# Kernel tuning notes

Hardware: AMD Instinct MI355X
Metric: run time of the kernel (lower is better)

## Reference

```python
import jax, jax.numpy as jnp
import numpy as np

B, T, D = 2, 2048, 512
HEADS, DIM_HEAD, MAX_LAG = 8, 64, 5
INNER = HEADS * DIM_HEAD


def setup_inputs() -> dict:
    key = jax.random.key(0)
    k0, k1, k2, k3, k4 = jax.random.split(key, 5)
    x = jax.random.normal(k0, (B, T, D), dtype=jnp.float32)
    # Linear weights stored as (in, out); torch applies x @ W.T with W (out, in).
    Wq = jax.random.normal(k1, (D, INNER), dtype=jnp.float32) * (1.0 / np.sqrt(D))
    Wk = jax.random.normal(k2, (D, INNER), dtype=jnp.float32) * (1.0 / np.sqrt(D))
    Wv = jax.random.normal(k3, (D, INNER), dtype=jnp.float32) * (1.0 / np.sqrt(D))
    Wo = jax.random.normal(k4, (INNER, D), dtype=jnp.float32) * (1.0 / np.sqrt(INNER))
    bo = jnp.zeros((D,), dtype=jnp.float32)
    # Module's init: lag_weights = log(exp(-lags/(max_lag/3))) = -lags/(max_lag/3)
    lags = jnp.arange(MAX_LAG + 1, dtype=jnp.float32)
    lag_weights = jnp.broadcast_to(-(lags / (MAX_LAG / 3.0)), (HEADS, MAX_LAG + 1)).astype(jnp.float32)
    return {"x": x, "Wq": Wq, "Wk": Wk, "Wv": Wv, "Wo": Wo, "bo": bo, "lag_weights": lag_weights}


def reference(x, Wq, Wk, Wv, Wo, bo, lag_weights):
    b, t, _ = x.shape
    h, dh = HEADS, DIM_HEAD
    scale = dh ** -0.5
    # context defaults to x (self-attention)
    q = (x @ Wq).reshape(b, t, h, dh).transpose(0, 2, 1, 3)  # b h t d
    k = (x @ Wk).reshape(b, t, h, dh).transpose(0, 2, 1, 3)
    v = (x @ Wv).reshape(b, t, h, dh).transpose(0, 2, 1, 3)
    sim = jnp.einsum('bhid,bhjd->bhij', q, k) * scale  # b h t t
    # causal mask: keep j <= i
    causal = jnp.tril(jnp.ones((t, t), dtype=bool))
    neg = -jnp.finfo(sim.dtype).max
    sim = jnp.where(causal[None, None], sim, neg)
    # learned additive time-lag bias: lag_adj[h,i,j] = softmax(lag_weights)[h, clamp(i-j,0,MAX_LAG)]
    ti = jnp.arange(t)
    time_lags = jnp.clip(ti[:, None] - ti[None, :], 0, MAX_LAG)  # t t
    lag_probs = jax.nn.softmax(lag_weights, axis=-1)  # h (L+1)
    lag_adj = lag_probs[:, time_lags]  # h t t
    sim = sim + lag_adj[None]
    attn = jax.nn.softmax(sim, axis=-1)
    out = jnp.einsum('bhij,bhjd->bhid', attn, v)
    out = out.transpose(0, 2, 1, 3).reshape(b, t, h * dh)  # b t inner
    return out @ Wo + bo  # dropout is identity at eval
```

## Files before the change

### kernel.cpp

```cpp
#include <hip/hip_runtime.h>
#include <hip/hip_bf16.h>

#define BB 2
#define TT 2048
#define DD 512
#define HH 8
#define DH 64
#define INNER 512
#define MAXLAG 5

typedef __attribute__((ext_vector_type(8))) short short8;
typedef __attribute__((ext_vector_type(4))) float floatx4;
typedef unsigned short ushort_t;

__device__ inline unsigned short f2bf(float f) {
    unsigned u = __float_as_uint(f);
    unsigned r = (u + 0x7FFFu + ((u >> 16) & 1u)) >> 16;
    return (unsigned short)r;
}
__device__ inline float bf2f(unsigned short u) {
    return __uint_as_float(((unsigned)u) << 16);
}

#define NXE (BB * TT * DD)

__global__ __launch_bounds__(256)
void cvt_kernel(const float* __restrict__ x,
                const float* __restrict__ wq, const float* __restrict__ wk,
                const float* __restrict__ wv, const float* __restrict__ wo,
                ushort_t* __restrict__ xb,
                ushort_t* __restrict__ wqt, ushort_t* __restrict__ wkt,
                ushort_t* __restrict__ wvt, ushort_t* __restrict__ wot)
{
    __shared__ float T[32][33];
    const int bid = blockIdx.x;
    if (bid < 1024) {
        int off = (bid * 256 + threadIdx.x) * 8;
        float4 a = *(const float4*)&x[off];
        float4 b = *(const float4*)&x[off + 4];
        ushort_t t[8];
        t[0] = f2bf(a.x); t[1] = f2bf(a.y); t[2] = f2bf(a.z); t[3] = f2bf(a.w);
        t[4] = f2bf(b.x); t[5] = f2bf(b.y); t[6] = f2bf(b.z); t[7] = f2bf(b.w);
        *(uint4*)&xb[off] = *(const uint4*)t;
        return;
    }
    const int r = bid - 1024;
    const int z = r >> 8;
    const int tile = r & 255;
    const float* s = (z == 0) ? wq : (z == 1) ? wk : (z == 2) ? wv : wo;
    ushort_t*    d = (z == 0) ? wqt : (z == 1) ? wkt : (z == 2) ? wvt : wot;
    const int k0 = (tile & 15) * 32;
    const int n0 = (tile >> 4) * 32;
    {
        const int kk = threadIdx.x >> 3;
        const int n4 = (threadIdx.x & 7) * 4;
        float4 v = *(const float4*)&s[(size_t)(k0 + kk) * 512 + n0 + n4];
        T[kk][n4 + 0] = v.x; T[kk][n4 + 1] = v.y;
        T[kk][n4 + 2] = v.z; T[kk][n4 + 3] = v.w;
    }
    __syncthreads();
    {
        const int nn = threadIdx.x >> 3;
        const int k4 = (threadIdx.x & 7) * 4;
        ushort4 o;
        o.x = f2bf(T[k4 + 0][nn]); o.y = f2bf(T[k4 + 1][nn]);
        o.z = f2bf(T[k4 + 2][nn]); o.w = f2bf(T[k4 + 3][nn]);
        *(ushort4*)&d[(size_t)(n0 + nn) * 512 + k0 + k4] = o;
    }
}

#define GM 64
#define GN 64
#define GK 32

template <typename OutT>
__global__ __launch_bounds__(256)
void gemm64(const ushort_t* __restrict__ A,
            const ushort_t* __restrict__ B0, const ushort_t* __restrict__ B1,
            const ushort_t* __restrict__ B2,
            OutT* __restrict__ O0, OutT* __restrict__ O1, OutT* __restrict__ O2,
            const float* __restrict__ bias, int M, int N, int K, int vtrans)
{
    const ushort_t* Bw = (blockIdx.z == 0) ? B0 : ((blockIdx.z == 1) ? B1 : B2);
    OutT*           O  = (blockIdx.z == 0) ? O0 : ((blockIdx.z == 1) ? O1 : O2);
    const int dotrans = vtrans && (blockIdx.z == 2);

    __shared__ ushort_t As[GM * GK];
    __shared__ ushort_t Bs[GN * GK];

    const int tid  = threadIdx.x;
    const int wave = tid >> 6;
    const int lane = tid & 63;
    const int quad = lane >> 4;
    const int l15  = lane & 15;
    const int wr   = wave >> 1;
    const int wc   = wave & 1;
    const int bm   = blockIdx.y * GM;
    const int bn   = blockIdx.x * GN;

    const ushort_t* ap = &A[(size_t)(bm + (tid >> 2)) * K + (tid & 3) * 8];
    const ushort_t* bp = &Bw[(size_t)(bn + (tid >> 2)) * K + (tid & 3) * 8];

    floatx4 acc[2][2];
#pragma unroll
    for (int i = 0; i < 2; ++i)
#pragma unroll
        for (int j = 0; j < 2; ++j) acc[i][j] = (floatx4){0.f, 0.f, 0.f, 0.f};

    uint4 pa = *(const uint4*)ap;
    uint4 pb = *(const uint4*)bp;

    for (int k0 = 0; k0 < K; k0 += GK) {
        __syncthreads();
        *(uint4*)&As[tid * 8] = pa;
        *(uint4*)&Bs[tid * 8] = pb;
        if (k0 + GK < K) {
            pa = *(const uint4*)(ap + k0 + GK);
            pb = *(const uint4*)(bp + k0 + GK);
        }
        __syncthreads();

        short8 af[2], bf[2];
#pragma unroll
        for (int mt = 0; mt < 2; ++mt)
            af[mt] = *(const short8*)&As[(((wr * 32 + mt * 16 + l15) << 2) + quad) * 8];
#pragma unroll
        for (int nt = 0; nt < 2; ++nt)
            bf[nt] = *(const short8*)&Bs[(((wc * 32 + nt * 16 + l15) << 2) + quad) * 8];
#pragma unroll
        for (int mt = 0; mt < 2; ++mt)
#pragma unroll
            for (int nt = 0; nt < 2; ++nt)
                acc[mt][nt] = __builtin_amdgcn_mfma_f32_16x16x32_bf16(
                    af[mt], bf[nt], acc[mt][nt], 0, 0, 0);
    }

    if (dotrans) {
#pragma unroll
        for (int mt = 0; mt < 2; ++mt) {
            const int m0 = bm + wr * 32 + mt * 16 + quad * 4;
            const int b  = m0 >> 11;
            const int t0 = m0 & 2047;
#pragma unroll
            for (int nt = 0; nt < 2; ++nt) {
                const int n = bn + wc * 32 + nt * 16 + l15;
                const int h = n >> 6, dd = n & 63;
                ushort4 o;
                o.x = f2bf(acc[mt][nt][0]); o.y = f2bf(acc[mt][nt][1]);
                o.z = f2bf(acc[mt][nt][2]); o.w = f2bf(acc[mt][nt][3]);
                *(ushort4*)&((ushort_t*)O)[((size_t)((b * 8 + h) * 64 + dd)) * 2048 + t0] = o;
            }
        }
        return;
    }

    float bv[2] = {0.f, 0.f};
    if (bias) {
#pragma unroll
        for (int nt = 0; nt < 2; ++nt)
            bv[nt] = bias[bn + wc * 32 + nt * 16 + l15];
    }
#pragma unroll
    for (int mt = 0; mt < 2; ++mt) {
#pragma unroll
        for (int nt = 0; nt < 2; ++nt) {
            const int n = bn + wc * 32 + nt * 16 + l15;
#pragma unroll
            for (int reg = 0; reg < 4; ++reg) {
                const int m = bm + wr * 32 + mt * 16 + quad * 4 + reg;
                float v = acc[mt][nt][reg] + bv[nt];
                if constexpr (sizeof(OutT) == 2)
                    O[(size_t)m * N + n] = (OutT)f2bf(v);
                else
                    O[(size_t)m * N + n] = (OutT)v;
            }
        }
    }
}

#define PAD 72
#define MFIX 10.0f

__global__ __launch_bounds__(256)
void attn_mfma(const ushort_t* __restrict__ Qg,
               const ushort_t* __restrict__ Kg,
               const ushort_t* __restrict__ Vtg,
               const float* __restrict__ lagw,
               ushort_t* __restrict__ Opart,
               float* __restrict__ Lpart)
{
    __shared__ ushort_t Ks[64 * 8 * 8];
    __shared__ ushort_t Vts[64 * 8 * 8];
    __shared__ ushort_t Pl[4][16][PAD];

    const int tid  = threadIdx.x;
    const int wave = tid >> 6;
    const int lane = tid & 63;
    const int quad = lane >> 4;
    const int l15  = lane & 15;

    const int bh = blockIdx.y;
    const int b  = bh >> 3;
    const int h  = bh & 7;
    const int c  = blockIdx.x;
    const int qt = 31 - (c >> 1);
    const int sp = c & 1;
    const int i0 = qt * 64;
    const int h1 = (qt + 1) >> 1;
    const int lo = sp ? h1 : 0;
    const int hi = sp ? (qt + 1) : h1;

    float lagb[MAXLAG + 1];
    {
        float mx = -1e30f;
#pragma unroll
        for (int l = 0; l <= MAXLAG; ++l) {
            lagb[l] = lagw[h * (MAXLAG + 1) + l];
            mx = fmaxf(mx, lagb[l]);
        }
        float s = 0.f;
#pragma unroll
        for (int l = 0; l <= MAXLAG; ++l) { lagb[l] = __expf(lagb[l] - mx); s += lagb[l]; }
        float inv = 1.f / s;
#pragma unroll
        for (int l = 0; l <= MAXLAG; ++l) lagb[l] = lagb[l] * inv - MFIX;
    }
    const float c1  = 0.125f;
    const float c2f = lagb[MAXLAG];

    short8 qf0, qf1;
    {
        const ushort_t* qbase =
            Qg + ((size_t)(b * TT + i0 + wave * 16 + l15)) * INNER + h * DH;
        qf0 = *(const short8*)(qbase + quad * 8);
        qf1 = *(const short8*)(qbase + 32 + quad * 8);
    }

    floatx4 oacc[4];
    float lsum[4] = {0.f, 0.f, 0.f, 0.f};
#pragma unroll
    for (int cb = 0; cb < 4; ++cb) oacc[cb] = (floatx4){0.f, 0.f, 0.f, 0.f};

    const int ibase = i0 + wave * 16 + quad * 4;

    const int srow = tid >> 3;
    const int sc   = tid & 7;
    const ushort_t* Kp0 = Kg + ((size_t)(b * TT) + srow) * INNER + h * DH + sc * 8;
    const ushort_t* Kp1 = Kp0 + (size_t)32 * INNER;
    const ushort_t* Vp0 = Vtg + ((size_t)(bh * 64 + srow)) * 2048 + sc * 8;
    const ushort_t* Vp1 = Vp0 + (size_t)32 * 2048;
    const int slot = (sc + srow) & 7;
    const int kdst0 = ((srow << 3) + slot) << 3;
    const int kdst1 = (((srow + 32) << 3) + slot) << 3;

    uint4 pk0, pk1, pv0, pv1;
    if (lo < hi) {
        const size_t koff = (size_t)(lo * 64) * INNER;
        pk0 = *(const uint4*)(Kp0 + koff);
        pk1 = *(const uint4*)(Kp1 + koff);
        pv0 = *(const uint4*)(Vp0 + lo * 64);
        pv1 = *(const uint4*)(Vp1 + lo * 64);
    }

    for (int kt = lo; kt < hi; ++kt) {
        __syncthreads();
        *(uint4*)&Ks[kdst0]  = pk0;
        *(uint4*)&Ks[kdst1]  = pk1;
        *(uint4*)&Vts[kdst0] = pv0;
        *(uint4*)&Vts[kdst1] = pv1;
        if (kt + 1 < hi) {
            const size_t koff = (size_t)((kt + 1) * 64) * INNER;
            pk0 = *(const uint4*)(Kp0 + koff);
            pk1 = *(const uint4*)(Kp1 + koff);
            pv0 = *(const uint4*)(Vp0 + (kt + 1) * 64);
            pv1 = *(const uint4*)(Vp1 + (kt + 1) * 64);
        }
        __syncthreads();

        const int j0 = kt * 64;

        floatx4 sacc[4];
#pragma unroll
        for (int cb = 0; cb < 4; ++cb) {
            const int key = cb * 16 + l15;
            short8 kf0 = *(const short8*)&Ks[((key << 3) + ((quad + key) & 7)) << 3];
            short8 kf1 = *(const short8*)&Ks[((key << 3) + ((quad + 4 + key) & 7)) << 3];
            floatx4 z = (floatx4){0.f, 0.f, 0.f, 0.f};
            z = __builtin_amdgcn_mfma_f32_16x16x32_bf16(qf0, kf0, z, 0, 0, 0);
            z = __builtin_amdgcn_mfma_f32_16x16x32_bf16(qf1, kf1, z, 0, 0, 0);
            sacc[cb] = z;
        }

        float p[4][4];
        if (i0 + wave * 16 - (j0 + 63) >= MAXLAG) {
#pragma unroll
            for (int cb = 0; cb < 4; ++cb)
#pragma unroll
                for (int reg = 0; reg < 4; ++reg)
                    p[cb][reg] = __expf(fmaf(sacc[cb][reg], c1, c2f));
        } else {
#pragma unroll
            for (int cb = 0; cb < 4; ++cb) {
                const int j = j0 + cb * 16 + l15;
#pragma unroll
                for (int reg = 0; reg < 4; ++reg) {
                    const int lag = (ibase + reg) - j;
                    float bias = (lag <= 0) ? lagb[0]
                               : (lag == 1) ? lagb[1]
                               : (lag == 2) ? lagb[2]
                               : (lag == 3) ? lagb[3]
                               : (lag == 4) ? lagb[4] : lagb[5];
                    float e = __expf(fmaf(sacc[cb][reg], c1, bias));
                    p[cb][reg] = (lag < 0) ? 0.f : e;
                }
            }
        }
#pragma unroll
        for (int cb = 0; cb < 4; ++cb)
#pragma unroll
            for (int reg = 0; reg < 4; ++reg)
                lsum[reg] += p[cb][reg];

#pragma unroll
        for (int cb = 0; cb < 4; ++cb)
#pragma unroll
            for (int reg = 0; reg < 4; ++reg)
                Pl[wave][quad * 4 + reg][cb * 16 + l15] = f2bf(p[cb][reg]);

        short8 pf0 = *(const short8*)&Pl[wave][l15][quad * 8];
        short8 pf1 = *(const short8*)&Pl[wave][l15][32 + quad * 8];

#pragma unroll
        for (int cb = 0; cb < 4; ++cb) {
            const int dd = cb * 16 + l15;
            short8 vf0 = *(const short8*)&Vts[((dd << 3) + ((quad + dd) & 7)) << 3];
            short8 vf1 = *(const short8*)&Vts[((dd << 3) + ((quad + 4 + dd) & 7)) << 3];
            oacc[cb] = __builtin_amdgcn_mfma_f32_16x16x32_bf16(pf0, vf0, oacc[cb], 0, 0, 0);
            oacc[cb] = __builtin_amdgcn_mfma_f32_16x16x32_bf16(pf1, vf1, oacc[cb], 0, 0, 0);
        }
    }

#pragma unroll
    for (int reg = 0; reg < 4; ++reg) {
        lsum[reg] += __shfl_xor(lsum[reg], 1);
        lsum[reg] += __shfl_xor(lsum[reg], 2);
        lsum[reg] += __shfl_xor(lsum[reg], 4);
        lsum[reg] += __shfl_xor(lsum[reg], 8);
    }

#pragma unroll
    for (int reg = 0; reg < 4; ++reg) {
        const int row = ibase + reg;
        const size_t obase = ((size_t)(sp * 16 + bh) * TT + row) * 64;
#pragma unroll
        for (int cb = 0; cb < 4; ++cb)
            Opart[obase + cb * 16 + l15] = f2bf(oacc[cb][reg]);
        if (l15 == 0)
            Lpart[(size_t)(sp * 16 + bh) * TT + row] = lsum[reg];
    }
}

#define CMB_UNITS (16 * TT * 16)

__global__ __launch_bounds__(256)
void combine_kernel(const ushort_t* __restrict__ Opart,
                    const float* __restrict__ Lpart,
                    ushort_t* __restrict__ ao)
{
    int u = blockIdx.x * 256 + threadIdx.x;
    const int bh  = u >> 15;
    const int rem = u & 32767;
    const int i   = rem >> 4;
    const int d   = (rem & 15) * 4;
    const int b   = bh >> 3;
    const int h   = bh & 7;

    const size_t p0 = ((size_t)bh * TT + i) * 64 + d;
    const size_t p1 = ((size_t)(16 + bh) * TT + i) * 64 + d;
    ushort4 a0 = *(const ushort4*)&Opart[p0];
    ushort4 a1 = *(const ushort4*)&Opart[p1];
    const float l = Lpart[(size_t)bh * TT + i] + Lpart[(size_t)(16 + bh) * TT + i];
    const float inv = 1.f / l;

    ushort4 o;
    o.x = f2bf((bf2f(a0.x) + bf2f(a1.x)) * inv);
    o.y = f2bf((bf2f(a0.y) + bf2f(a1.y)) * inv);
    o.z = f2bf((bf2f(a0.z) + bf2f(a1.z)) * inv);
    o.w = f2bf((bf2f(a0.w) + bf2f(a1.w)) * inv);
    *(ushort4*)&ao[((size_t)(b * TT + i)) * INNER + h * DH + d] = o;
}

extern "C" void kernel_launch(void* const* d_in, const int* in_sizes, int n_in,
                              void* d_out, int out_size, void* d_ws, size_t ws_size,
                              hipStream_t stream)
{
    const float* x  = (const float*)d_in[0];
    const float* Wq = (const float*)d_in[1];
    const float* Wk = (const float*)d_in[2];
    const float* Wv = (const float*)d_in[3];
    const float* Wo = (const float*)d_in[4];
    const float* bo = (const float*)d_in[5];
    const float* lw = (const float*)d_in[6];
    float* out = (float*)d_out;

    const size_t SZ  = (size_t)BB * TT * INNER;
    const size_t NWE = (size_t)DD * INNER;
    ushort_t* xb    = (ushort_t*)d_ws;
    ushort_t* wqt   = xb + SZ;
    ushort_t* wkt   = wqt + NWE;
    ushort_t* wvt   = wkt + NWE;
    ushort_t* wot   = wvt + NWE;
    ushort_t* q     = wot + NWE;
    ushort_t* k     = q + SZ;
    ushort_t* vt    = k + SZ;
    ushort_t* opart = vt + SZ;
    float*    lpart = (float*)(opart + 2 * SZ);
    ushort_t* ao    = xb;

    const int M = BB * TT;

    cvt_kernel<<<2048, 256, 0, stream>>>(x, Wq, Wk, Wv, Wo,
                                         xb, wqt, wkt, wvt, wot);

    dim3 gQKV(INNER / GN, M / GM, 3);
    gemm64<ushort_t><<<gQKV, 256, 0, stream>>>(
        xb, wqt, wkt, wvt, q, k, vt, nullptr, M, INNER, DD, 1);

    dim3 gATT(64, BB * HH);
    attn_mfma<<<gATT, 256, 0, stream>>>(q, k, vt, lw, opart, lpart);

    combine_kernel<<<CMB_UNITS / 256, 256, 0, stream>>>(opart, lpart, ao);

    dim3 gPRJ(DD / GN, M / GM, 1);
    gemm64<float><<<gPRJ, 256, 0, stream>>>(
        ao, wot, wot, wot, out, out, out, bo, M, DD, INNER, 0);
}
```

Measured before the change: 138.6 us.

## Load K and V fragments directly from global memory, dropping LDS staging

The attention kernel stops staging K and V tiles through shared memory. Each wave now reads its MFMA operand fragments straight from global memory, prefetching the next K tile into registers and loading V at the start of each iteration. This removes the two block barriers per key tile and the LDS round trip. In exchange, every one of the four waves loads the same K/V data redundantly, relying on cache, and register pressure rises.

```diff
diff --git a/kernel.cpp b/kernel.cpp
--- a/kernel.cpp
+++ b/kernel.cpp
@@ -21,8 +21,6 @@
 __device__ inline float bf2f(unsigned short u) {
     return __uint_as_float(((unsigned)u) << 16);
 }
-
-#define NXE (BB * TT * DD)
 
 __global__ __launch_bounds__(256)
 void cvt_kernel(const float* __restrict__ x,
@@ -189,8 +187,6 @@
                ushort_t* __restrict__ Opart,
                float* __restrict__ Lpart)
 {
-    __shared__ ushort_t Ks[64 * 8 * 8];
-    __shared__ ushort_t Vts[64 * 8 * 8];
     __shared__ ushort_t Pl[4][16][PAD];
 
     const int tid  = threadIdx.x;
@@ -243,51 +239,51 @@
 
     const int ibase = i0 + wave * 16 + quad * 4;
 
-    const int srow = tid >> 3;
-    const int sc   = tid & 7;
-    const ushort_t* Kp0 = Kg + ((size_t)(b * TT) + srow) * INNER + h * DH + sc * 8;
-    const ushort_t* Kp1 = Kp0 + (size_t)32 * INNER;
-    const ushort_t* Vp0 = Vtg + ((size_t)(bh * 64 + srow)) * 2048 + sc * 8;
-    const ushort_t* Vp1 = Vp0 + (size_t)32 * 2048;
-    const int slot = (sc + srow) & 7;
-    const int kdst0 = ((srow << 3) + slot) << 3;
-    const int kdst1 = (((srow + 32) << 3) + slot) << 3;
-
-    uint4 pk0, pk1, pv0, pv1;
+    const ushort_t* Kb = Kg + ((size_t)b * TT) * INNER + h * DH;
+    const ushort_t* Vb = Vtg + ((size_t)bh * 64) * TT;
+
+    size_t koff[4], voff[4];
+#pragma unroll
+    for (int cb = 0; cb < 4; ++cb) {
+        koff[cb] = (size_t)(cb * 16 + l15) * INNER + quad * 8;
+        voff[cb] = (size_t)(cb * 16 + l15) * TT + quad * 8;
+    }
+
+    short8 ka0[4], ka1[4];
     if (lo < hi) {
-        const size_t koff = (size_t)(lo * 64) * INNER;
-        pk0 = *(const uint4*)(Kp0 + koff);
-        pk1 = *(const uint4*)(Kp1 + koff);
-        pv0 = *(const uint4*)(Vp0 + lo * 64);
-        pv1 = *(const uint4*)(Vp1 + lo * 64);
+        const size_t j0e = (size_t)(lo * 64) * INNER;
+#pragma unroll
+        for (int cb = 0; cb < 4; ++cb) {
+            ka0[cb] = *(const short8*)(Kb + j0e + koff[cb]);
+            ka1[cb] = *(const short8*)(Kb + j0e + koff[cb] + 32);
+        }
     }
 
     for (int kt = lo; kt < hi; ++kt) {
-        __syncthreads();
-        *(uint4*)&Ks[kdst0]  = pk0;
-        *(uint4*)&Ks[kdst1]  = pk1;
-        *(uint4*)&Vts[kdst0] = pv0;
-        *(uint4*)&Vts[kdst1] = pv1;
+        const int j0 = kt * 64;
+
+        short8 vv0[4], vv1[4];
+#pragma unroll
+        for (int cb = 0; cb < 4; ++cb) {
+            vv0[cb] = *(const short8*)(Vb + voff[cb] + j0);
+            vv1[cb] = *(const short8*)(Vb + voff[cb] + j0 + 32);
+        }
+        short8 kn0[4], kn1[4];
         if (kt + 1 < hi) {
-            const size_t koff = (size_t)((kt + 1) * 64) * INNER;
-            pk0 = *(const uint4*)(Kp0 + koff);
-            pk1 = *(const uint4*)(Kp1 + koff);
-            pv0 = *(const uint4*)(Vp0 + (kt + 1) * 64);
-            pv1 = *(const uint4*)(Vp1 + (kt + 1) * 64);
-        }
-        __syncthreads();
-
-        const int j0 = kt * 64;
+            const size_t jn = (size_t)(j0 + 64) * INNER;
+#pragma unroll
+            for (int cb = 0; cb < 4; ++cb) {
+                kn0[cb] = *(const short8*)(Kb + jn + koff[cb]);
+                kn1[cb] = *(const short8*)(Kb + jn + koff[cb] + 32);
+            }
+        }
 
         floatx4 sacc[4];
 #pragma unroll
         for (int cb = 0; cb < 4; ++cb) {
-            const int key = cb * 16 + l15;
-            short8 kf0 = *(const short8*)&Ks[((key << 3) + ((quad + key) & 7)) << 3];
-            short8 kf1 = *(const short8*)&Ks[((key << 3) + ((quad + 4 + key) & 7)) << 3];
             floatx4 z = (floatx4){0.f, 0.f, 0.f, 0.f};
-            z = __builtin_amdgcn_mfma_f32_16x16x32_bf16(qf0, kf0, z, 0, 0, 0);
-            z = __builtin_amdgcn_mfma_f32_16x16x32_bf16(qf1, kf1, z, 0, 0, 0);
+            z = __builtin_amdgcn_mfma_f32_16x16x32_bf16(qf0, ka0[cb], z, 0, 0, 0);
+            z = __builtin_amdgcn_mfma_f32_16x16x32_bf16(qf1, ka1[cb], z, 0, 0, 0);
             sacc[cb] = z;
         }
 
@@ -332,12 +328,12 @@
 
 #pragma unroll
         for (int cb = 0; cb < 4; ++cb) {
-            const int dd = cb * 16 + l15;
-            short8 vf0 = *(const short8*)&Vts[((dd << 3) + ((quad + dd) & 7)) << 3];
-            short8 vf1 = *(const short8*)&Vts[((dd << 3) + ((quad + 4 + dd) & 7)) << 3];
-            oacc[cb] = __builtin_amdgcn_mfma_f32_16x16x32_bf16(pf0, vf0, oacc[cb], 0, 0, 0);
-            oacc[cb] = __builtin_amdgcn_mfma_f32_16x16x32_bf16(pf1, vf1, oacc[cb], 0, 0, 0);
-        }
+            oacc[cb] = __builtin_amdgcn_mfma_f32_16x16x32_bf16(pf0, vv0[cb], oacc[cb], 0, 0, 0);
+            oacc[cb] = __builtin_amdgcn_mfma_f32_16x16x32_bf16(pf1, vv1[cb], oacc[cb], 0, 0, 0);
+        }
+
+#pragma unroll
+        for (int cb = 0; cb < 4; ++cb) { ka0[cb] = kn0[cb]; ka1[cb] = kn1[cb]; }
     }
 
 #pragma unroll
```

New measurement: 212.7 us. +53.5%, slower.

## Fuse split-K attention combine into output projection and enlarge GEMM tiles

Applied to the files above, without the earlier changes.

The separate combine kernel is removed. The output projection GEMM now reads both partial attention outputs, normalizes them with the summed softmax denominators while staging the A tile, and applies bias at the end. Both the QKV and projection GEMMs move from 64x64x32 tiles to 128x128x64 tiles, with 16 accumulators per wave. This saves one launch and an intermediate round trip through memory. The cost is fewer blocks: 384 for QKV and only 128 for the projection, which may underfill the GPU, plus extra loads in the projection's staging step.

```diff
diff --git a/kernel.cpp b/kernel.cpp
--- a/kernel.cpp
+++ b/kernel.cpp
@@ -21,8 +21,6 @@
 __device__ inline float bf2f(unsigned short u) {
     return __uint_as_float(((unsigned)u) << 16);
 }
-
-#define NXE (BB * TT * DD)
 
 __global__ __launch_bounds__(256)
 void cvt_kernel(const float* __restrict__ x,
@@ -69,24 +67,24 @@
     }
 }
 
-#define GM 64
-#define GN 64
-#define GK 32
-
-template <typename OutT>
+#define QBM 128
+#define QBN 128
+#define QBK 64
+
 __global__ __launch_bounds__(256)
-void gemm64(const ushort_t* __restrict__ A,
+void qkv128(const ushort_t* __restrict__ A,
             const ushort_t* __restrict__ B0, const ushort_t* __restrict__ B1,
             const ushort_t* __restrict__ B2,
-            OutT* __restrict__ O0, OutT* __restrict__ O1, OutT* __restrict__ O2,
-            const float* __restrict__ bias, int M, int N, int K, int vtrans)
+            ushort_t* __restrict__ O0, ushort_t* __restrict__ O1,
+            ushort_t* __restrict__ O2)
 {
     const ushort_t* Bw = (blockIdx.z == 0) ? B0 : ((blockIdx.z == 1) ? B1 : B2);
-    OutT*           O  = (blockIdx.z == 0) ? O0 : ((blockIdx.z == 1) ? O1 : O2);
-    const int dotrans = vtrans && (blockIdx.z == 2);
-
-    __shared__ ushort_t As[GM * GK];
-    __shared__ ushort_t Bs[GN * GK];
+    ushort_t*       O  = (blockIdx.z == 0) ? O0 : ((blockIdx.z == 1) ? O1 : O2);
+    const int dotrans = (blockIdx.z == 2);
+    const int K = DD;
+
+    __shared__ ushort_t As[QBM * QBK];
+    __shared__ ushort_t Bs[QBN * QBK];
 
     const int tid  = threadIdx.x;
     const int wave = tid >> 6;
@@ -95,84 +93,91 @@
     const int l15  = lane & 15;
     const int wr   = wave >> 1;
     const int wc   = wave & 1;
-    const int bm   = blockIdx.y * GM;
-    const int bn   = blockIdx.x * GN;
-
-    const ushort_t* ap = &A[(size_t)(bm + (tid >> 2)) * K + (tid & 3) * 8];
-    const ushort_t* bp = &Bw[(size_t)(bn + (tid >> 2)) * K + (tid & 3) * 8];
-
-    floatx4 acc[2][2];
-#pragma unroll
-    for (int i = 0; i < 2; ++i)
-#pragma unroll
-        for (int j = 0; j < 2; ++j) acc[i][j] = (floatx4){0.f, 0.f, 0.f, 0.f};
-
-    uint4 pa = *(const uint4*)ap;
-    uint4 pb = *(const uint4*)bp;
-
-    for (int k0 = 0; k0 < K; k0 += GK) {
+    const int bm   = blockIdx.y * QBM;
+    const int bn   = blockIdx.x * QBN;
+
+    const int sr  = tid >> 3;
+    const int sc8 = (tid & 7) * 8;
+    const ushort_t* ap[4];
+    const ushort_t* bp[4];
+#pragma unroll
+    for (int i = 0; i < 4; ++i) {
+        ap[i] = &A[(size_t)(bm + sr + 32 * i) * K + sc8];
+        bp[i] = &Bw[(size_t)(bn + sr + 32 * i) * K + sc8];
+    }
+
+    floatx4 acc[4][4];
+#pragma unroll
+    for (int i = 0; i < 4; ++i)
+#pragma unroll
+        for (int j = 0; j < 4; ++j) acc[i][j] = (floatx4){0.f, 0.f, 0.f, 0.f};
+
+    uint4 pa[4], pb[4];
+#pragma unroll
+    for (int i = 0; i < 4; ++i) { pa[i] = *(const uint4*)ap[i]; pb[i] = *(const uint4*)bp[i]; }
+
+    for (int k0 = 0; k0 < K; k0 += QBK) {
         __syncthreads();
-        *(uint4*)&As[tid * 8] = pa;
-        *(uint4*)&Bs[tid * 8] = pb;
-        if (k0 + GK < K) {
-            pa = *(const uint4*)(ap + k0 + GK);
-            pb = *(const uint4*)(bp + k0 + GK);
+#pragma unroll
+        for (int i = 0; i < 4; ++i) {
+            *(uint4*)&As[(tid + 256 * i) * 8] = pa[i];
+            *(uint4*)&Bs[(tid + 256 * i) * 8] = pb[i];
+        }
+        if (k0 + QBK < K) {
+#pragma unroll
+            for (int i = 0; i < 4; ++i) {
+                pa[i] = *(const uint4*)(ap[i] + k0 + QBK);
+                pb[i] = *(const uint4*)(bp[i] + k0 + QBK);
+            }
         }
         __syncthreads();
 
-        short8 af[2], bf[2];
-#pragma unroll
-        for (int mt = 0; mt < 2; ++mt)
-            af[mt] = *(const short8*)&As[(((wr * 32 + mt * 16 + l15) << 2) + quad) * 8];
-#pragma unroll
-        for (int nt = 0; nt < 2; ++nt)
-            bf[nt] = *(const short8*)&Bs[(((wc * 32 + nt * 16 + l15) << 2) + quad) * 8];
-#pragma unroll
-        for (int mt = 0; mt < 2; ++mt)
-#pragma unroll
-            for (int nt = 0; nt < 2; ++nt)
-                acc[mt][nt] = __builtin_amdgcn_mfma_f32_16x16x32_bf16(
-                    af[mt], bf[nt], acc[mt][nt], 0, 0, 0);
+#pragma unroll
+        for (int ks = 0; ks < 2; ++ks) {
+            short8 af[4], bf[4];
+#pragma unroll
+            for (int mt = 0; mt < 4; ++mt)
+                af[mt] = *(const short8*)&As[(((wr * 64 + mt * 16 + l15) << 3) + ks * 4 + quad) * 8];
+#pragma unroll
+            for (int nt = 0; nt < 4; ++nt)
+                bf[nt] = *(const short8*)&Bs[(((wc * 64 + nt * 16 + l15) << 3) + ks * 4 + quad) * 8];
+#pragma unroll
+            for (int mt = 0; mt < 4; ++mt)
+#pragma unroll
+                for (int nt = 0; nt < 4; ++nt)
+                    acc[mt][nt] = __builtin_amdgcn_mfma_f32_16x16x32_bf16(
+                        af[mt], bf[nt], acc[mt][nt], 0, 0, 0);
+        }
     }
 
     if (dotrans) {
 #pragma unroll
-        for (int mt = 0; mt < 2; ++mt) {
-            const int m0 = bm + wr * 32 + mt * 16 + quad * 4;
+        for (int mt = 0; mt < 4; ++mt) {
+            const int m0 = bm + wr * 64 + mt * 16 + quad * 4;
             const int b  = m0 >> 11;
             const int t0 = m0 & 2047;
 #pragma unroll
-            for (int nt = 0; nt < 2; ++nt) {
-                const int n = bn + wc * 32 + nt * 16 + l15;
+            for (int nt = 0; nt < 4; ++nt) {
+                const int n = bn + wc * 64 + nt * 16 + l15;
                 const int h = n >> 6, dd = n & 63;
                 ushort4 o;
                 o.x = f2bf(acc[mt][nt][0]); o.y = f2bf(acc[mt][nt][1]);
                 o.z = f2bf(acc[mt][nt][2]); o.w = f2bf(acc[mt][nt][3]);
-                *(ushort4*)&((ushort_t*)O)[((size_t)((b * 8 + h) * 64 + dd)) * 2048 + t0] = o;
+                *(ushort4*)&O[((size_t)((b * 8 + h) * 64 + dd)) * 2048 + t0] = o;
             }
         }
         return;
     }
 
-    float bv[2] = {0.f, 0.f};
-    if (bias) {
-#pragma unroll
-        for (int nt = 0; nt < 2; ++nt)
-            bv[nt] = bias[bn + wc * 32 + nt * 16 + l15];
-    }
-#pragma unroll
-    for (int mt = 0; mt < 2; ++mt) {
-#pragma unroll
-        for (int nt = 0; nt < 2; ++nt) {
-            const int n = bn + wc * 32 + nt * 16 + l15;
+#pragma unroll
+    for (int mt = 0; mt < 4; ++mt) {
+#pragma unroll
+        for (int nt = 0; nt < 4; ++nt) {
+            const int n = bn + wc * 64 + nt * 16 + l15;
 #pragma unroll
             for (int reg = 0; reg < 4; ++reg) {
-                const int m = bm + wr * 32 + mt * 16 + quad * 4 + reg;
-                float v = acc[mt][nt][reg] + bv[nt];
-                if constexpr (sizeof(OutT) == 2)
-                    O[(size_t)m * N + n] = (OutT)f2bf(v);
-                else
-                    O[(size_t)m * N + n] = (OutT)v;
+                const int m = bm + wr * 64 + mt * 16 + quad * 4 + reg;
+                O[(size_t)m * INNER + n] = f2bf(acc[mt][nt][reg]);
             }
         }
     }
@@ -360,34 +365,127 @@
     }
 }
 
-#define CMB_UNITS (16 * TT * 16)
-
 __global__ __launch_bounds__(256)
-void combine_kernel(const ushort_t* __restrict__ Opart,
-                    const float* __restrict__ Lpart,
-                    ushort_t* __restrict__ ao)
+void proj128(const ushort_t* __restrict__ Opart,
+             const float* __restrict__ Lpart,
+             const ushort_t* __restrict__ Bw,
+             const float* __restrict__ bias,
+             float* __restrict__ O)
 {
-    int u = blockIdx.x * 256 + threadIdx.x;
-    const int bh  = u >> 15;
-    const int rem = u & 32767;
-    const int i   = rem >> 4;
-    const int d   = (rem & 15) * 4;
-    const int b   = bh >> 3;
-    const int h   = bh & 7;
-
-    const size_t p0 = ((size_t)bh * TT + i) * 64 + d;
-    const size_t p1 = ((size_t)(16 + bh) * TT + i) * 64 + d;
-    ushort4 a0 = *(const ushort4*)&Opart[p0];
-    ushort4 a1 = *(const ushort4*)&Opart[p1];
-    const float l = Lpart[(size_t)bh * TT + i] + Lpart[(size_t)(16 + bh) * TT + i];
-    const float inv = 1.f / l;
-
-    ushort4 o;
-    o.x = f2bf((bf2f(a0.x) + bf2f(a1.x)) * inv);
-    o.y = f2bf((bf2f(a0.y) + bf2f(a1.y)) * inv);
-    o.z = f2bf((bf2f(a0.z) + bf2f(a1.z)) * inv);
-    o.w = f2bf((bf2f(a0.w) + bf2f(a1.w)) * inv);
-    *(ushort4*)&ao[((size_t)(b * TT + i)) * INNER + h * DH + d] = o;
+    const int K = INNER;
+
+    __shared__ ushort_t As[QBM * QBK];
+    __shared__ ushort_t Bs[QBN * QBK];
+    __shared__ float Linv[8 * 128];
+
+    const int tid  = threadIdx.x;
+    const int wave = tid >> 6;
+    const int lane = tid & 63;
+    const int quad = lane >> 4;
+    const int l15  = lane & 15;
+    const int wr   = wave >> 1;
+    const int wc   = wave & 1;
+    const int bm   = blockIdx.y * QBM;
+    const int bn   = blockIdx.x * QBN;
+
+    const int bblk  = bm >> 11;
+    const int tbase = bm & 2047;
+
+#pragma unroll
+    for (int i = 0; i < 4; ++i) {
+        const int idx = tid + 256 * i;
+        const int h = idx >> 7, r = idx & 127;
+        const size_t p = (size_t)(bblk * 8 + h) * 2048 + tbase + r;
+        Linv[idx] = 1.f / (Lpart[p] + Lpart[(size_t)16 * 2048 + p]);
+    }
+
+    const int sr  = tid >> 3;
+    const int sc8 = (tid & 7) * 8;
+    size_t aoff[4];
+#pragma unroll
+    for (int i = 0; i < 4; ++i)
+        aoff[i] = ((size_t)(bblk * 8) * 2048 + (tbase + sr + 32 * i)) * 64 + sc8;
+    const size_t SLOT = (size_t)16 * 2048 * 64;
+    const size_t HSTEP = (size_t)2048 * 64;
+
+    const ushort_t* bp[4];
+#pragma unroll
+    for (int i = 0; i < 4; ++i)
+        bp[i] = &Bw[(size_t)(bn + sr + 32 * i) * K + sc8];
+
+    floatx4 acc[4][4];
+#pragma unroll
+    for (int i = 0; i < 4; ++i)
+#pragma unroll
+        for (int j = 0; j < 4; ++j) acc[i][j] = (floatx4){0.f, 0.f, 0.f, 0.f};
+
+    uint4 pa0[4], pa1[4], pb[4];
+#pragma unroll
+    for (int i = 0; i < 4; ++i) {
+        pa0[i] = *(const uint4*)&Opart[aoff[i]];
+        pa1[i] = *(const uint4*)&Opart[aoff[i] + SLOT];
+        pb[i]  = *(const uint4*)bp[i];
+    }
+
+    for (int k0 = 0; k0 < K; k0 += QBK) {
+        const int h = k0 >> 6;
+        __syncthreads();
+#pragma unroll
+        for (int i = 0; i < 4; ++i) {
+            const float inv = Linv[h * 128 + sr + 32 * i];
+            const ushort_t* a0 = (const ushort_t*)&pa0[i];
+            const ushort_t* a1 = (const ushort_t*)&pa1[i];
+            ushort_t t[8];
+#pragma unroll
+            for (int j = 0; j < 8; ++j)
+                t[j] = f2bf((bf2f(a0[j]) + bf2f(a1[j])) * inv);
+            *(uint4*)&As[(tid + 256 * i) * 8] = *(const uint4*)t;
+            *(uint4*)&Bs[(tid + 256 * i) * 8] = pb[i];
+        }
+        if (k0 + QBK < K) {
+#pragma unroll
+            for (int i = 0; i < 4; ++i) {
+                pa0[i] = *(const uint4*)&Opart[aoff[i] + HSTEP * (h + 1)];
+                pa1[i] = *(const uint4*)&Opart[aoff[i] + HSTEP * (h + 1) + SLOT];
+                pb[i]  = *(const uint4*)(bp[i] + k0 + QBK);
+            }
+        }
+        __syncthreads();
+
+#pragma unroll
+        for (int ks = 0; ks < 2; ++ks) {
+            short8 af[4], bf[4];
+#pragma unroll
+            for (int mt = 0; mt < 4; ++mt)
+                af[mt] = *(const short8*)&As[(((wr * 64 + mt * 16 + l15) << 3) + ks * 4 + quad) * 8];
+#pragma unroll
+            for (int nt = 0; nt < 4; ++nt)
+                bf[nt] = *(const short8*)&Bs[(((wc * 64 + nt * 16 + l15) << 3) + ks * 4 + quad) * 8];
+#pragma unroll
+            for (int mt = 0; mt < 4; ++mt)
+#pragma unroll
+                for (int nt = 0; nt < 4; ++nt)
+                    acc[mt][nt] = __builtin_amdgcn_mfma_f32_16x16x32_bf16(
+                        af[mt], bf[nt], acc[mt][nt], 0, 0, 0);
+        }
+    }
+
+    float bv[4];
+#pragma unroll
+    for (int nt = 0; nt < 4; ++nt)
+        bv[nt] = bias[bn + wc * 64 + nt * 16 + l15];
+#pragma unroll
+    for (int mt = 0; mt < 4; ++mt) {
+#pragma unroll
+        for (int nt = 0; nt < 4; ++nt) {
+            const int n = bn + wc * 64 + nt * 16 + l15;
+#pragma unroll
+            for (int reg = 0; reg < 4; ++reg) {
+                const int m = bm + wr * 64 + mt * 16 + quad * 4 + reg;
+                O[(size_t)m * DD + n] = acc[mt][nt][reg] + bv[nt];
+            }
+        }
+    }
 }
 
 extern "C" void kernel_launch(void* const* d_in, const int* in_sizes, int n_in,
@@ -415,23 +513,18 @@
     ushort_t* vt    = k + SZ;
     ushort_t* opart = vt + SZ;
     float*    lpart = (float*)(opart + 2 * SZ);
-    ushort_t* ao    = xb;
 
     const int M = BB * TT;
 
     cvt_kernel<<<2048, 256, 0, stream>>>(x, Wq, Wk, Wv, Wo,
                                          xb, wqt, wkt, wvt, wot);
 
-    dim3 gQKV(INNER / GN, M / GM, 3);
-    gemm64<ushort_t><<<gQKV, 256, 0, stream>>>(
-        xb, wqt, wkt, wvt, q, k, vt, nullptr, M, INNER, DD, 1);
+    dim3 gQKV(INNER / QBN, M / QBM, 3);
+    qkv128<<<gQKV, 256, 0, stream>>>(xb, wqt, wkt, wvt, q, k, vt);
 
     dim3 gATT(64, BB * HH);
     attn_mfma<<<gATT, 256, 0, stream>>>(q, k, vt, lw, opart, lpart);
 
-    combine_kernel<<<CMB_UNITS / 256, 256, 0, stream>>>(opart, lpart, ao);
-
-    dim3 gPRJ(DD / GN, M / GM, 1);
-    gemm64<float><<<gPRJ, 256, 0, stream>>>(
-        ao, wot, wot, wot, out, out, out, bo, M, DD, INNER, 0);
-}
+    dim3 gPRJ(DD / QBN, M / QBM);
+    proj128<<<gPRJ, 256, 0, stream>>>(opart, lpart, wot, bo, out);
+}
```

New measurement: 174.1 us. 1.26x slower.

## Fuse split-K combine into output projection and tile V-transpose layout

Applied to the files above, without the earlier changes.

Removes the separate combine kernel: the output-projection GEMM now reads both attention partial outputs and partial sums directly, normalizes and sums them while staging the A tile, then runs the MFMA GEMM with bias. V transposed output is stored in 64x64 key-tile blocks so each attention tile load is contiguous. It also specializes the QKV GEMM with compile-time K. This saves a launch and an intermediate write/read round trip. In exchange, the projection reads two partial buffers per tile, and each of the 8 column blocks redoes the normalization work.

```diff
diff --git a/kernel.cpp b/kernel.cpp
--- a/kernel.cpp
+++ b/kernel.cpp
@@ -21,8 +21,6 @@
 __device__ inline float bf2f(unsigned short u) {
     return __uint_as_float(((unsigned)u) << 16);
 }
-
-#define NXE (BB * TT * DD)
 
 __global__ __launch_bounds__(256)
 void cvt_kernel(const float* __restrict__ x,
@@ -73,17 +71,17 @@
 #define GN 64
 #define GK 32
 
-template <typename OutT>
 __global__ __launch_bounds__(256)
-void gemm64(const ushort_t* __restrict__ A,
-            const ushort_t* __restrict__ B0, const ushort_t* __restrict__ B1,
-            const ushort_t* __restrict__ B2,
-            OutT* __restrict__ O0, OutT* __restrict__ O1, OutT* __restrict__ O2,
-            const float* __restrict__ bias, int M, int N, int K, int vtrans)
+void qkv64(const ushort_t* __restrict__ A,
+           const ushort_t* __restrict__ B0, const ushort_t* __restrict__ B1,
+           const ushort_t* __restrict__ B2,
+           ushort_t* __restrict__ O0, ushort_t* __restrict__ O1,
+           ushort_t* __restrict__ O2)
 {
     const ushort_t* Bw = (blockIdx.z == 0) ? B0 : ((blockIdx.z == 1) ? B1 : B2);
-    OutT*           O  = (blockIdx.z == 0) ? O0 : ((blockIdx.z == 1) ? O1 : O2);
-    const int dotrans = vtrans && (blockIdx.z == 2);
+    ushort_t*       O  = (blockIdx.z == 0) ? O0 : ((blockIdx.z == 1) ? O1 : O2);
+    const int dotrans = (blockIdx.z == 2);
+    const int K = DD;
 
     __shared__ ushort_t As[GM * GK];
     __shared__ ushort_t Bs[GN * GK];
@@ -141,6 +139,8 @@
             const int m0 = bm + wr * 32 + mt * 16 + quad * 4;
             const int b  = m0 >> 11;
             const int t0 = m0 & 2047;
+            const int kt = t0 >> 6;
+            const int tl = t0 & 63;
 #pragma unroll
             for (int nt = 0; nt < 2; ++nt) {
                 const int n = bn + wc * 32 + nt * 16 + l15;
@@ -148,18 +148,12 @@
                 ushort4 o;
                 o.x = f2bf(acc[mt][nt][0]); o.y = f2bf(acc[mt][nt][1]);
                 o.z = f2bf(acc[mt][nt][2]); o.w = f2bf(acc[mt][nt][3]);
-                *(ushort4*)&((ushort_t*)O)[((size_t)((b * 8 + h) * 64 + dd)) * 2048 + t0] = o;
+                *(ushort4*)&O[(((size_t)((b * 8 + h) * 32 + kt)) * 64 + dd) * 64 + tl] = o;
             }
         }
         return;
     }
 
-    float bv[2] = {0.f, 0.f};
-    if (bias) {
-#pragma unroll
-        for (int nt = 0; nt < 2; ++nt)
-            bv[nt] = bias[bn + wc * 32 + nt * 16 + l15];
-    }
 #pragma unroll
     for (int mt = 0; mt < 2; ++mt) {
 #pragma unroll
@@ -168,11 +162,7 @@
 #pragma unroll
             for (int reg = 0; reg < 4; ++reg) {
                 const int m = bm + wr * 32 + mt * 16 + quad * 4 + reg;
-                float v = acc[mt][nt][reg] + bv[nt];
-                if constexpr (sizeof(OutT) == 2)
-                    O[(size_t)m * N + n] = (OutT)f2bf(v);
-                else
-                    O[(size_t)m * N + n] = (OutT)v;
+                O[(size_t)m * INNER + n] = f2bf(acc[mt][nt][reg]);
             }
         }
     }
@@ -247,8 +237,8 @@
     const int sc   = tid & 7;
     const ushort_t* Kp0 = Kg + ((size_t)(b * TT) + srow) * INNER + h * DH + sc * 8;
     const ushort_t* Kp1 = Kp0 + (size_t)32 * INNER;
-    const ushort_t* Vp0 = Vtg + ((size_t)(bh * 64 + srow)) * 2048 + sc * 8;
-    const ushort_t* Vp1 = Vp0 + (size_t)32 * 2048;
+    const ushort_t* Vp0 = Vtg + ((size_t)bh * 32 * 64 + srow) * 64 + sc * 8;
+    const ushort_t* Vp1 = Vp0 + 32 * 64;
     const int slot = (sc + srow) & 7;
     const int kdst0 = ((srow << 3) + slot) << 3;
     const int kdst1 = (((srow + 32) << 3) + slot) << 3;
@@ -258,8 +248,8 @@
         const size_t koff = (size_t)(lo * 64) * INNER;
         pk0 = *(const uint4*)(Kp0 + koff);
         pk1 = *(const uint4*)(Kp1 + koff);
-        pv0 = *(const uint4*)(Vp0 + lo * 64);
-        pv1 = *(const uint4*)(Vp1 + lo * 64);
+        pv0 = *(const uint4*)(Vp0 + lo * 4096);
+        pv1 = *(const uint4*)(Vp1 + lo * 4096);
     }
 
     for (int kt = lo; kt < hi; ++kt) {
@@ -272,8 +262,8 @@
             const size_t koff = (size_t)((kt + 1) * 64) * INNER;
             pk0 = *(const uint4*)(Kp0 + koff);
             pk1 = *(const uint4*)(Kp1 + koff);
-            pv0 = *(const uint4*)(Vp0 + (kt + 1) * 64);
-            pv1 = *(const uint4*)(Vp1 + (kt + 1) * 64);
+            pv0 = *(const uint4*)(Vp0 + (kt + 1) * 4096);
+            pv1 = *(const uint4*)(Vp1 + (kt + 1) * 4096);
         }
         __syncthreads();
 
@@ -360,34 +350,113 @@
     }
 }
 
-#define CMB_UNITS (16 * TT * 16)
-
 __global__ __launch_bounds__(256)
-void combine_kernel(const ushort_t* __restrict__ Opart,
-                    const float* __restrict__ Lpart,
-                    ushort_t* __restrict__ ao)
+void proj64(const ushort_t* __restrict__ Opart,
+            const float* __restrict__ Lpart,
+            const ushort_t* __restrict__ Bw,
+            const float* __restrict__ bias,
+            float* __restrict__ O)
 {
-    int u = blockIdx.x * 256 + threadIdx.x;
-    const int bh  = u >> 15;
-    const int rem = u & 32767;
-    const int i   = rem >> 4;
-    const int d   = (rem & 15) * 4;
-    const int b   = bh >> 3;
-    const int h   = bh & 7;
-
-    const size_t p0 = ((size_t)bh * TT + i) * 64 + d;
-    const size_t p1 = ((size_t)(16 + bh) * TT + i) * 64 + d;
-    ushort4 a0 = *(const ushort4*)&Opart[p0];
-    ushort4 a1 = *(const ushort4*)&Opart[p1];
-    const float l = Lpart[(size_t)bh * TT + i] + Lpart[(size_t)(16 + bh) * TT + i];
-    const float inv = 1.f / l;
-
-    ushort4 o;
-    o.x = f2bf((bf2f(a0.x) + bf2f(a1.x)) * inv);
-    o.y = f2bf((bf2f(a0.y) + bf2f(a1.y)) * inv);
-    o.z = f2bf((bf2f(a0.z) + bf2f(a1.z)) * inv);
-    o.w = f2bf((bf2f(a0.w) + bf2f(a1.w)) * inv);
-    *(ushort4*)&ao[((size_t)(b * TT + i)) * INNER + h * DH + d] = o;
+    const int K = INNER;
+
+    __shared__ ushort_t As[GM * GK];
+    __shared__ ushort_t Bs[GN * GK];
+    __shared__ float Linv[8 * 64];
+
+    const int tid  = threadIdx.x;
+    const int wave = tid >> 6;
+    const int lane = tid & 63;
+    const int quad = lane >> 4;
+    const int l15  = lane & 15;
+    const int wr   = wave >> 1;
+    const int wc   = wave & 1;
+    const int bm   = blockIdx.y * GM;
+    const int bn   = blockIdx.x * GN;
+
+    const int bblk  = bm >> 11;
+    const int tbase = bm & 2047;
+
+    {
+        const int i1 = tid;
+        const size_t p1 = (size_t)(bblk * 8 + (i1 >> 6)) * 2048 + tbase + (i1 & 63);
+        Linv[i1] = 1.f / (Lpart[p1] + Lpart[(size_t)16 * 2048 + p1]);
+        const int i2 = tid + 256;
+        const size_t p2 = (size_t)(bblk * 8 + (i2 >> 6)) * 2048 + tbase + (i2 & 63);
+        Linv[i2] = 1.f / (Lpart[p2] + Lpart[(size_t)16 * 2048 + p2]);
+    }
+
+    const int sr  = tid >> 2;
+    const int sc8 = (tid & 3) * 8;
+    const size_t abase = ((size_t)(bblk * 8) * 2048 + tbase + sr) * 64 + sc8;
+    const size_t HSTEP = (size_t)2048 * 64;
+    const size_t SLOT  = (size_t)16 * 2048 * 64;
+
+    const ushort_t* bp = &Bw[(size_t)(bn + sr) * K + sc8];
+
+    floatx4 acc[2][2];
+#pragma unroll
+    for (int i = 0; i < 2; ++i)
+#pragma unroll
+        for (int j = 0; j < 2; ++j) acc[i][j] = (floatx4){0.f, 0.f, 0.f, 0.f};
+
+    uint4 pa0 = *(const uint4*)&Opart[abase];
+    uint4 pa1 = *(const uint4*)&Opart[abase + SLOT];
+    uint4 pb  = *(const uint4*)bp;
+
+    for (int k0 = 0; k0 < K; k0 += GK) {
+        const int h = k0 >> 6;
+        __syncthreads();
+        {
+            const float inv = Linv[h * 64 + sr];
+            const ushort_t* a0 = (const ushort_t*)&pa0;
+            const ushort_t* a1 = (const ushort_t*)&pa1;
+            ushort_t t[8];
+#pragma unroll
+            for (int j = 0; j < 8; ++j)
+                t[j] = f2bf((bf2f(a0[j]) + bf2f(a1[j])) * inv);
+            *(uint4*)&As[tid * 8] = *(const uint4*)t;
+            *(uint4*)&Bs[tid * 8] = pb;
+        }
+        if (k0 + GK < K) {
+            const int kn = k0 + GK;
+            const size_t aoff = abase + HSTEP * (kn >> 6) + (kn & 32);
+            pa0 = *(const uint4*)&Opart[aoff];
+            pa1 = *(const uint4*)&Opart[aoff + SLOT];
+            pb  = *(const uint4*)(bp + kn);
+        }
+        __syncthreads();
+
+        short8 af[2], bf[2];
+#pragma unroll
+        for (int mt = 0; mt < 2; ++mt)
+            af[mt] = *(const short8*)&As[(((wr * 32 + mt * 16 + l15) << 2) + quad) * 8];
+#pragma unroll
+        for (int nt = 0; nt < 2; ++nt)
+            bf[nt] = *(const short8*)&Bs[(((wc * 32 + nt * 16 + l15) << 2) + quad) * 8];
+#pragma unroll
+        for (int mt = 0; mt < 2; ++mt)
+#pragma unroll
+            for (int nt = 0; nt < 2; ++nt)
+                acc[mt][nt] = __builtin_amdgcn_mfma_f32_16x16x32_bf16(
+                    af[mt], bf[nt], acc[mt][nt], 0, 0, 0);
+    }
+
+    float bv[2];
+#pragma unroll
+    for (int nt = 0; nt < 2; ++nt)
+        bv[nt] = bias[bn + wc * 32 + nt * 16 + l15];
+#pragma unroll
+    for (int mt = 0; mt < 2; ++mt) {
+#pragma unroll
+        for (int nt = 0; nt < 2; ++nt) {
+            const int n = bn + wc * 32 + nt * 16 + l15;
+#pragma unroll
+            for (int reg = 0; reg < 4; ++reg) {
+                const int m = bm + wr * 32 + mt * 16 + quad * 4 + reg;
+                O[(size_t)m * DD + n] = acc[mt][nt][reg] + bv[nt];
+            }
+        }
+    }
 }
 
 extern "C" void kernel_launch(void* const* d_in, const int* in_sizes, int n_in,
@@ -415,7 +484,6 @@
     ushort_t* vt    = k + SZ;
     ushort_t* opart = vt + SZ;
     float*    lpart = (float*)(opart + 2 * SZ);
-    ushort_t* ao    = xb;
 
     const int M = BB * TT;
 
@@ -423,15 +491,11 @@
                                          xb, wqt, wkt, wvt, wot);
 
     dim3 gQKV(INNER / GN, M / GM, 3);
-    gemm64<ushort_t><<<gQKV, 256, 0, stream>>>(
-        xb, wqt, wkt, wvt, q, k, vt, nullptr, M, INNER, DD, 1);
+    qkv64<<<gQKV, 256, 0, stream>>>(xb, wqt, wkt, wvt, q, k, vt);
 
     dim3 gATT(64, BB * HH);
     attn_mfma<<<gATT, 256, 0, stream>>>(q, k, vt, lw, opart, lpart);
 
-    combine_kernel<<<CMB_UNITS / 256, 256, 0, stream>>>(opart, lpart, ao);
-
-    dim3 gPRJ(DD / GN, M / GM, 1);
-    gemm64<float><<<gPRJ, 256, 0, stream>>>(
-        ao, wot, wot, wot, out, out, out, bo, M, DD, INNER, 0);
-}
+    dim3 gPRJ(DD / GN, M / GM);
+    proj64<<<gPRJ, 256, 0, stream>>>(opart, lpart, wot, bo, out);
+}
```

Measured after the change: 139.1 us. No clear change (+0.3%).
